# Optimization experiments

Hardware: AMD Instinct MI355X
Metric: run time of the kernel (lower is better)

## Reference

```python
import jax, jax.numpy as jnp
import numpy as np

HIDDEN = 1024
HEADS = 16
HEAD_DIM = HIDDEN // HEADS


def setup_inputs() -> dict:
    key = jax.random.key(0)
    ks = jax.random.split(key, 9)
    s = 1.0 / np.sqrt(HIDDEN)
    x = jax.random.normal(ks[0], (2, 2048, HIDDEN), dtype=jnp.float32)
    Wq = jax.random.uniform(ks[1], (HIDDEN, HIDDEN), jnp.float32, -s, s)
    bq = jax.random.uniform(ks[2], (HIDDEN,), jnp.float32, -s, s)
    Wk = jax.random.uniform(ks[3], (HIDDEN, HIDDEN), jnp.float32, -s, s)
    bk = jax.random.uniform(ks[4], (HIDDEN,), jnp.float32, -s, s)
    Wv = jax.random.uniform(ks[5], (HIDDEN, HIDDEN), jnp.float32, -s, s)
    bv = jax.random.uniform(ks[6], (HIDDEN,), jnp.float32, -s, s)
    Wo = jax.random.uniform(ks[7], (HIDDEN, HIDDEN), jnp.float32, -s, s)
    bo = jax.random.uniform(ks[8], (HIDDEN,), jnp.float32, -s, s)
    return {"x": x, "Wq": Wq, "bq": bq, "Wk": Wk, "bk": bk,
            "Wv": Wv, "bv": bv, "Wo": Wo, "bo": bo}


def reference(x, Wq, bq, Wk, bk, Wv, bv, Wo, bo):
    bs, seq_len, _ = x.shape
    # projections; weights stored as (in, out) so y = x @ W + b
    def proj(W, b):
        y = x @ W + b  # [bs, seq, hidden]
        return y.reshape(bs, seq_len, HEADS, HEAD_DIM).transpose(0, 2, 1, 3)  # [bs, h, seq, hd]
    q = proj(Wq, bq)
    k = proj(Wk, bk)
    v = proj(Wv, bv)
    scale = 1.0 / jnp.sqrt(jnp.float32(HEAD_DIM))
    scores = jnp.einsum('bhqd,bhkd->bhqk', q, k) * scale  # [bs, h, seq, seq]
    attn = jax.nn.softmax(scores, axis=-1)
    ctx = jnp.einsum('bhqk,bhkd->bhqd', attn, v)
    ctx = ctx.transpose(0, 2, 1, 3).reshape(bs, seq_len, HIDDEN)
    return ctx @ Wo + bo
```

## Files before the change

kernel.cpp:

```cpp
#include <hip/hip_runtime.h>
#include <hip/hip_bf16.h>

#define HDN 1024
#define NH  16
#define DH  64
#define NB  2
#define SQL 2048
#define MT  (NB*SQL)

using bf16 = __hip_bfloat16;
typedef __attribute__((ext_vector_type(8))) short s16x8;
typedef __attribute__((ext_vector_type(4))) float f32x4;
typedef __attribute__((ext_vector_type(16))) float f32x16;
typedef unsigned int u32;

#define QSC 0.18033688011112042f

__device__ __forceinline__ void gload_lds16(const void* g, void* l) {
  __builtin_amdgcn_global_load_lds((const __attribute__((address_space(1))) void*)g,
                                   (__attribute__((address_space(3))) void*)l, 16, 0, 0);
}

__device__ __forceinline__ unsigned short bfb(float f) {
  union { __hip_bfloat16 h; unsigned short u; } c;
  c.h = __float2bfloat16(f);
  return c.u;
}

__device__ __forceinline__ u32 cvtpk(float lo, float hi) {
  u32 r;
  asm("v_cvt_pk_bf16_f32 %0, %1, %2" : "=v"(r) : "v"(lo), "v"(hi));
  return r;
}

__device__ __forceinline__ void pl32swap(u32& a, u32& b) {
  asm("v_permlane32_swap_b32 %0, %1" : "+v"(a), "+v"(b));
}

__global__ __launch_bounds__(256) void k_cvt_x(const float* __restrict__ x, bf16* __restrict__ xb) {
  int i = (blockIdx.x * 256 + threadIdx.x) * 8;
  float4 a = *(const float4*)(x + i);
  float4 b = *(const float4*)(x + i + 4);
  union { unsigned short u[8]; uint4 v; } o;
  o.u[0]=bfb(a.x); o.u[1]=bfb(a.y); o.u[2]=bfb(a.z); o.u[3]=bfb(a.w);
  o.u[4]=bfb(b.x); o.u[5]=bfb(b.y); o.u[6]=bfb(b.z); o.u[7]=bfb(b.w);
  *(uint4*)((unsigned short*)xb + i) = o.v;
}

__global__ __launch_bounds__(256) void k_trw(const float* __restrict__ Wq, const float* __restrict__ Wk,
                                             const float* __restrict__ Wv, const float* __restrict__ Wo,
                                             bf16* __restrict__ WqkvT, bf16* __restrict__ WoT) {
  __shared__ float tile[64][65];
  int z = blockIdx.z;
  const float* W = (z==0)?Wq:(z==1)?Wk:(z==2)?Wv:Wo;
  bf16* Wt = (z<3) ? (WqkvT + (size_t)z*HDN*HDN) : WoT;
  int r0 = blockIdx.y*64, c0 = blockIdx.x*64;
  int t = threadIdx.x, tr = t>>4, tc = (t&15)*4;
  #pragma unroll
  for (int p=0;p<4;p++){
    int r = p*16+tr;
    float4 v = *(const float4*)(W + (size_t)(r0+r)*HDN + c0 + tc);
    tile[r][tc]=v.x; tile[r][tc+1]=v.y; tile[r][tc+2]=v.z; tile[r][tc+3]=v.w;
  }
  __syncthreads();
  #pragma unroll
  for (int p=0;p<4;p++){
    int o = p*16+tr;
    union { unsigned short u[4]; ushort4 v; } pk;
    #pragma unroll
    for (int j=0;j<4;j++) pk.u[j] = bfb(tile[tc+j][o]);
    *(ushort4*)((unsigned short*)Wt + (size_t)(c0+o)*HDN + r0 + tc) = pk.v;
  }
}

template<int MODE>
__global__ __launch_bounds__(256,2) void k_gemm(
    const bf16* __restrict__ A, const bf16* __restrict__ B,
    const float* __restrict__ b0, const float* __restrict__ b1, const float* __restrict__ b2,
    bf16* __restrict__ oq, bf16* __restrict__ ok, bf16* __restrict__ ovt, float* __restrict__ oo) {
  constexpr int KD = 1024;
  __shared__ __align__(16) char smem[34816];
  bf16* As = (bf16*)smem;
  bf16* Bs = (bf16*)(smem + 16384);
  int tid = threadIdx.x, lane = tid&63, wave = tid>>6;
  int g = lane>>4, lr = lane&15;

  int lin = blockIdx.y * gridDim.x + blockIdx.x;
  int nwg = gridDim.x * gridDim.y;
  int wg  = (lin & 7) * (nwg >> 3) + (lin >> 3);
  int bx  = wg % gridDim.x, by = wg / gridDim.x;

  int m0 = by*128, n0 = bx*128;
  int wm = (wave>>1)*64, wn = (wave&1)*64;
  f32x4 acc[4][4] = {};
  for (int k0=0; k0<KD; k0+=64) {
    #pragma unroll
    for (int i=0;i<4;i++){
      int seg = wave*4+i;
      int flat = seg*64 + lane;
      int row = flat>>3, ch = flat&7;
      gload_lds16(A + (size_t)(m0+row)*KD + k0 + ch*8, (char*)As + seg*1024);
      gload_lds16(B + (size_t)(n0+row)*KD + k0 + ch*8, (char*)Bs + seg*1024);
    }
    __syncthreads();
    #pragma unroll
    for (int kk=0;kk<2;kk++){
      s16x8 af[4], bfg[4];
      #pragma unroll
      for (int mi=0;mi<4;mi++)
        af[mi] = *(const s16x8*)((const char*)As + (wm+mi*16+lr)*128 + kk*64 + g*16);
      #pragma unroll
      for (int ni=0;ni<4;ni++)
        bfg[ni] = *(const s16x8*)((const char*)Bs + (wn+ni*16+lr)*128 + kk*64 + g*16);
      #pragma unroll
      for (int mi=0;mi<4;mi++)
        #pragma unroll
        for (int ni=0;ni<4;ni++)
          acc[mi][ni] = __builtin_amdgcn_mfma_f32_16x16x32_bf16(af[mi], bfg[ni], acc[mi][ni], 0,0,0);
    }
    __syncthreads();
  }
  if (MODE == 0) {
    int proj = n0 >> 10;
    if (proj < 2) {
      const float* bias = (proj==0)?b0:b1;
      bf16* oqk = (proj==0)?oq:ok;
      float qscale = (proj==0) ? QSC : 1.0f;
      #pragma unroll
      for (int ni=0;ni<4;ni++){
        int n = n0 + wn + ni*16 + lr;
        int wi = n & 1023;
        int h = wi>>6, d = wi&63;
        float bv = bias[wi];
        #pragma unroll
        for (int mi=0;mi<4;mi++){
          #pragma unroll
          for (int r=0;r<4;r++){
            int m = m0 + wm + mi*16 + g*4 + r;
            int b = m>>11, s = m&2047;
            float v = (acc[mi][ni][r] + bv) * qscale;
            oqk[((size_t)((b*NH+h)*SQL + s))*DH + d] = __float2bfloat16(v);
          }
        }
      }
    } else {
      #pragma unroll
      for (int ni=0;ni<4;ni++){
        int nl = wn + ni*16 + lr;
        float bv = b2[(n0 & 1023) + nl];
        #pragma unroll
        for (int mi=0;mi<4;mi++){
          #pragma unroll
          for (int rp=0; rp<4; rp+=2){
            int ml = wm + mi*16 + g*4 + rp;
            u32 pkd = (u32)bfb(acc[mi][ni][rp] + bv) | ((u32)bfb(acc[mi][ni][rp+1] + bv) << 16);
            *(u32*)(smem + nl*272 + ml*2) = pkd;
          }
        }
      }
      __syncthreads();
      int bb = m0 >> 11;
      #pragma unroll
      for (int it=0; it<8; ++it){
        int flat = it*256 + tid;
        int row = flat>>4, chk = flat&15;
        s16x8 val = *(const s16x8*)(smem + row*272 + chk*16);
        int wi = (n0 & 1023) + row;
        int hh = wi>>6, dd = wi&63;
        int ss = (m0 & 2047) + chk*8;
        *(s16x8*)(ovt + ((size_t)((bb*NH+hh)*DH + dd))*SQL + ss) = val;
      }
    }
  } else {
    #pragma unroll
    for (int ni=0;ni<4;ni++){
      int n = n0 + wn + ni*16 + lr;
      float bv = b0[n];
      #pragma unroll
      for (int mi=0;mi<4;mi++)
        #pragma unroll
        for (int r=0;r<4;r++){
          int m = m0 + wm + mi*16 + g*4 + r;
          oo[(size_t)m*HDN + n] = acc[mi][ni][r] + bv;
        }
    }
  }
}

__global__ __launch_bounds__(512,4) void k_attn(
    const bf16* __restrict__ Q, const bf16* __restrict__ K, const bf16* __restrict__ Vt,
    bf16* __restrict__ ctx) {
  __shared__ __align__(16) char sm[2][2][16384];
  int bh = blockIdx.x & 31, qt = blockIdx.x >> 5;
  int b = bh >> 4, h = bh & 15;
  int tid = threadIdx.x;
  int kc = tid >> 8, tl = tid & 255;
  int w4 = tl >> 6;
  int lane = tid & 63;
  int cl = lane & 31, hi = lane >> 5;
  const char* Kc = (const char*)(K  + (size_t)bh*SQL*DH);
  const char* Vc = (const char*)(Vt + (size_t)bh*DH*SQL);
  const bf16* Qb = Q + (size_t)bh*SQL*DH;

  int L0 = tl*16, L1 = 4096 + tl*16;
  int r0 = L0>>7, c0 = (L0&127) ^ ((r0&7)<<4);
  int r1 = L1>>7, c1 = (L1&127) ^ ((r1&7)<<4);
  size_t kOff0 = (size_t)r0*128  + c0, kOff1 = (size_t)r1*128  + c1;
  size_t vOff0 = (size_t)r0*4096 + c0, vOff1 = (size_t)r1*4096 + c1;

  int swz = (cl&7)<<4;
  int cswz0 = (0*32 + hi*16) ^ swz;
  int cswz1 = (1*32 + hi*16) ^ swz;
  int cswz2 = (2*32 + hi*16) ^ swz;
  int cswz3 = (3*32 + hi*16) ^ swz;
  int rbase0 = cl*128;
  int rbase1 = (32+cl)*128;

  int q0 = qt*128 + w4*32;
  s16x8 qf[4];
  #pragma unroll
  for (int ds=0; ds<4; ++ds)
    qf[ds] = *(const s16x8*)((const char*)Qb + (size_t)(q0+cl)*128 + ds*32 + hi*16);

  s16x8 onef;
  #pragma unroll
  for (int i=0;i<8;i++) onef[i] = (short)0x3F80;

  f32x16 ca0 = {}, ca1 = {}, lacc = {};

  auto STAGE = [&](int bb, int t){
    int k0 = kc*1024 + t*64;
    char* bK = &sm[kc][bb][0]; char* bV = bK + 8192;
    gload_lds16(Kc + (size_t)k0*128 + kOff0, bK + w4*1024);
    gload_lds16(Kc + (size_t)k0*128 + kOff1, bK + 4096 + w4*1024);
    gload_lds16(Vc + (size_t)k0*2   + vOff0, bV + w4*1024);
    gload_lds16(Vc + (size_t)k0*2   + vOff1, bV + 4096 + w4*1024);
  };

  STAGE(0, 0);
  __syncthreads();

  for (int t=0; t<16; ++t){
    int cur = t & 1;
    if (t < 15) STAGE(cur^1, t+1);
    const char* bK = &sm[kc][cur][0];
    const char* bV = bK + 8192;

    f32x16 s0 = {}, s1 = {};
    __builtin_amdgcn_s_setprio(1);
    {
      s16x8 k00 = *(const s16x8*)(bK + rbase0 + cswz0);
      s16x8 k10 = *(const s16x8*)(bK + rbase1 + cswz0);
      s0 = __builtin_amdgcn_mfma_f32_32x32x16_bf16(k00, qf[0], s0, 0,0,0);
      s1 = __builtin_amdgcn_mfma_f32_32x32x16_bf16(k10, qf[0], s1, 0,0,0);
      s16x8 k01 = *(const s16x8*)(bK + rbase0 + cswz1);
      s16x8 k11 = *(const s16x8*)(bK + rbase1 + cswz1);
      s0 = __builtin_amdgcn_mfma_f32_32x32x16_bf16(k01, qf[1], s0, 0,0,0);
      s1 = __builtin_amdgcn_mfma_f32_32x32x16_bf16(k11, qf[1], s1, 0,0,0);
      s16x8 k02 = *(const s16x8*)(bK + rbase0 + cswz2);
      s16x8 k12 = *(const s16x8*)(bK + rbase1 + cswz2);
      s0 = __builtin_amdgcn_mfma_f32_32x32x16_bf16(k02, qf[2], s0, 0,0,0);
      s1 = __builtin_amdgcn_mfma_f32_32x32x16_bf16(k12, qf[2], s1, 0,0,0);
      s16x8 k03 = *(const s16x8*)(bK + rbase0 + cswz3);
      s16x8 k13 = *(const s16x8*)(bK + rbase1 + cswz3);
      s0 = __builtin_amdgcn_mfma_f32_32x32x16_bf16(k03, qf[3], s0, 0,0,0);
      s1 = __builtin_amdgcn_mfma_f32_32x32x16_bf16(k13, qf[3], s1, 0,0,0);
    }
    __builtin_amdgcn_s_setprio(0);

    s16x8 pf[4];
    #pragma unroll
    for (int kb=0; kb<2; ++kb){
      float e[16];
      #pragma unroll
      for (int i=0;i<16;i++) e[i] = exp2f(kb ? s1[i] : s0[i]);
      u32 w00=cvtpk(e[0],e[1]),   w01=cvtpk(e[2],e[3]);
      u32 w10=cvtpk(e[4],e[5]),   w11=cvtpk(e[6],e[7]);
      u32 w20=cvtpk(e[8],e[9]),   w21=cvtpk(e[10],e[11]);
      u32 w30=cvtpk(e[12],e[13]), w31=cvtpk(e[14],e[15]);
      pl32swap(w00, w10);
      pl32swap(w01, w11);
      pl32swap(w20, w30);
      pl32swap(w21, w31);
      union { u32 u[4]; s16x8 v; } A, B;
      A.u[0]=w00; A.u[1]=w01; A.u[2]=w10; A.u[3]=w11;
      B.u[0]=w20; B.u[1]=w21; B.u[2]=w30; B.u[3]=w31;
      pf[kb*2]   = A.v;
      pf[kb*2+1] = B.v;
    }

    __builtin_amdgcn_s_setprio(1);
    {
      s16x8 v00 = *(const s16x8*)(bV + rbase0 + cswz0);
      s16x8 v10 = *(const s16x8*)(bV + rbase1 + cswz0);
      ca0 = __builtin_amdgcn_mfma_f32_32x32x16_bf16(v00, pf[0], ca0, 0,0,0);
      ca1 = __builtin_amdgcn_mfma_f32_32x32x16_bf16(v10, pf[0], ca1, 0,0,0);
      lacc = __builtin_amdgcn_mfma_f32_32x32x16_bf16(onef, pf[0], lacc, 0,0,0);
      s16x8 v01 = *(const s16x8*)(bV + rbase0 + cswz1);
      s16x8 v11 = *(const s16x8*)(bV + rbase1 + cswz1);
      ca0 = __builtin_amdgcn_mfma_f32_32x32x16_bf16(v01, pf[1], ca0, 0,0,0);
      ca1 = __builtin_amdgcn_mfma_f32_32x32x16_bf16(v11, pf[1], ca1, 0,0,0);
      lacc = __builtin_amdgcn_mfma_f32_32x32x16_bf16(onef, pf[1], lacc, 0,0,0);
      s16x8 v02 = *(const s16x8*)(bV + rbase0 + cswz2);
      s16x8 v12 = *(const s16x8*)(bV + rbase1 + cswz2);
      ca0 = __builtin_amdgcn_mfma_f32_32x32x16_bf16(v02, pf[2], ca0, 0,0,0);
      ca1 = __builtin_amdgcn_mfma_f32_32x32x16_bf16(v12, pf[2], ca1, 0,0,0);
      lacc = __builtin_amdgcn_mfma_f32_32x32x16_bf16(onef, pf[2], lacc, 0,0,0);
      s16x8 v03 = *(const s16x8*)(bV + rbase0 + cswz3);
      s16x8 v13 = *(const s16x8*)(bV + rbase1 + cswz3);
      ca0 = __builtin_amdgcn_mfma_f32_32x32x16_bf16(v03, pf[3], ca0, 0,0,0);
      ca1 = __builtin_amdgcn_mfma_f32_32x32x16_bf16(v13, pf[3], ca1, 0,0,0);
      lacc = __builtin_amdgcn_mfma_f32_32x32x16_bf16(onef, pf[3], lacc, 0,0,0);
    }
    __builtin_amdgcn_s_setprio(0);
    __syncthreads();
  }

  float lrow = lacc[0];

  char*  base = &sm[0][0][0];
  float* lb   = (float*)(base + 16384);
  float* o2b  = (float*)(base + 32768);
  char*  cb   = base;

  __syncthreads();
  if (kc == 1) {
    if (!hi) lb[w4*32+cl] = lrow;
    #pragma unroll
    for (int db=0; db<2; ++db)
      #pragma unroll
      for (int r=0; r<16; ++r){
        int d = db*32 + (r&3) + 8*(r>>2) + 4*hi;
        o2b[w4*2048 + d*32 + cl] = db ? ca1[r] : ca0[r];
      }
  }
  __syncthreads();
  if (kc == 0) {
    float inv = 1.f / (lrow + lb[w4*32+cl]);
    int row = w4*32 + cl;
    int rswz = (row&7)<<4;
    #pragma unroll
    for (int db=0; db<2; ++db){
      #pragma unroll
      for (int r=0; r<16; r+=2){
        int d = db*32 + (r&3) + 8*(r>>2) + 4*hi;
        float va = ((db?ca1[r]:ca0[r])     + o2b[w4*2048 + d*32     + cl]) * inv;
        float vb = ((db?ca1[r+1]:ca0[r+1]) + o2b[w4*2048 + (d+1)*32 + cl]) * inv;
        *(u32*)(cb + row*128 + ((d*2) ^ rswz)) = cvtpk(va, vb);
      }
    }
  }
  __syncthreads();
  if (kc == 0) {
    #pragma unroll
    for (int i=0;i<4;i++){
      int flat = i*256 + tl, orow = flat>>3, ch = flat&7;
      s16x8 cv = *(const s16x8*)(cb + orow*128 + ((ch*16) ^ ((orow&7)<<4)));
      *(s16x8*)(ctx + (size_t)(b*SQL + qt*128 + orow)*HDN + h*DH + ch*8) = cv;
    }
  }
}

extern "C" void kernel_launch(void* const* d_in, const int* in_sizes, int n_in,
                              void* d_out, int out_size, void* d_ws, size_t ws_size,
                              hipStream_t stream) {
  const float* x  = (const float*)d_in[0];
  const float* Wq = (const float*)d_in[1];
  const float* bq = (const float*)d_in[2];
  const float* Wk = (const float*)d_in[3];
  const float* bk = (const float*)d_in[4];
  const float* Wv = (const float*)d_in[5];
  const float* bv = (const float*)d_in[6];
  const float* Wo = (const float*)d_in[7];
  const float* bo = (const float*)d_in[8];
  char* ws = (char*)d_ws;
  bf16* xb    = (bf16*)(ws);
  bf16* WqkvT = (bf16*)(ws + ((size_t)8<<20));
  bf16* WoT   = (bf16*)(ws + ((size_t)14<<20));
  bf16* Qg    = (bf16*)(ws + ((size_t)16<<20));
  bf16* Kg    = (bf16*)(ws + ((size_t)24<<20));
  bf16* Vtg   = (bf16*)(ws + ((size_t)32<<20));
  bf16* Ctx   = (bf16*)(ws + ((size_t)40<<20));
  float* out  = (float*)d_out;

  k_cvt_x<<<2048, 256, 0, stream>>>(x, xb);
  k_trw<<<dim3(16,16,4), 256, 0, stream>>>(Wq, Wk, Wv, Wo, WqkvT, WoT);
  k_gemm<0><<<dim3(24,32), 256, 0, stream>>>(xb, WqkvT, bq, bk, bv, Qg, Kg, Vtg, nullptr);
  k_attn<<<512, 512, 0, stream>>>(Qg, Kg, Vtg, Ctx);
  k_gemm<1><<<dim3(8,32), 256, 0, stream>>>(Ctx, WoT, bo, nullptr, nullptr,
                                            nullptr, nullptr, nullptr, out);
}
```

Measured before the change: 197.6 us.

## Give each attention wave two Q subtiles, drop ones-MFMA row sums, stage QK epilogue

The attention kernel shrinks to 256 threads, with each wave handling 64 query rows as two 32-row subtiles that share every loaded K/V fragment. This halves LDS fragment reads per MFMA. The ones-matrix MFMA used for row sums is replaced by scalar accumulation of the exponentials plus a cross-half shuffle. Separately, the Q/K projection epilogue now goes through shared memory so it can issue 16-byte coalesced stores instead of scattered 2-byte stores, and the GEMM launch bound asks for 3 blocks per CU. The costs are higher register pressure in attention and fewer threads per block to hide latency.

```diff
diff --git a/kernel.cpp b/kernel.cpp
--- a/kernel.cpp
+++ b/kernel.cpp
@@ -74,7 +74,7 @@
 }
 
 template<int MODE>
-__global__ __launch_bounds__(256,2) void k_gemm(
+__global__ __launch_bounds__(256,3) void k_gemm(
     const bf16* __restrict__ A, const bf16* __restrict__ B,
     const float* __restrict__ b0, const float* __restrict__ b1, const float* __restrict__ b2,
     bf16* __restrict__ oq, bf16* __restrict__ ok, bf16* __restrict__ ovt, float* __restrict__ oo) {
@@ -128,20 +128,27 @@
       float qscale = (proj==0) ? QSC : 1.0f;
       #pragma unroll
       for (int ni=0;ni<4;ni++){
-        int n = n0 + wn + ni*16 + lr;
-        int wi = n & 1023;
-        int h = wi>>6, d = wi&63;
-        float bv = bias[wi];
-        #pragma unroll
-        for (int mi=0;mi<4;mi++){
+        int nl = wn + ni*16 + lr;
+        float bv = bias[(n0&1023) + nl];
+        #pragma unroll
+        for (int mi=0;mi<4;mi++)
           #pragma unroll
           for (int r=0;r<4;r++){
-            int m = m0 + wm + mi*16 + g*4 + r;
-            int b = m>>11, s = m&2047;
-            float v = (acc[mi][ni][r] + bv) * qscale;
-            oqk[((size_t)((b*NH+h)*SQL + s))*DH + d] = __float2bfloat16(v);
+            int ml = wm + mi*16 + g*4 + r;
+            *(unsigned short*)(smem + ml*272 + nl*2) = bfb((acc[mi][ni][r] + bv) * qscale);
           }
-        }
+      }
+      __syncthreads();
+      int bb = m0 >> 11;
+      int h0 = (n0 & 1023) >> 6;
+      #pragma unroll
+      for (int it=0; it<8; ++it){
+        int flat = it*256 + tid;
+        int row = flat>>4, chk = flat&15;
+        s16x8 val = *(const s16x8*)(smem + row*272 + chk*16);
+        int s = (m0 & 2047) + row;
+        int hh = h0 + (chk>>3), dd = (chk&7)*8;
+        *(s16x8*)(oqk + ((size_t)((bb*NH+hh)*SQL + s))*DH + dd) = val;
       }
     } else {
       #pragma unroll
@@ -187,26 +194,25 @@
   }
 }
 
-__global__ __launch_bounds__(512,4) void k_attn(
+__global__ __launch_bounds__(256,2) void k_attn(
     const bf16* __restrict__ Q, const bf16* __restrict__ K, const bf16* __restrict__ Vt,
     bf16* __restrict__ ctx) {
   __shared__ __align__(16) char sm[2][2][16384];
   int bh = blockIdx.x & 31, qt = blockIdx.x >> 5;
   int b = bh >> 4, h = bh & 15;
   int tid = threadIdx.x;
-  int kc = tid >> 8, tl = tid & 255;
-  int w4 = tl >> 6;
+  int kc = tid >> 7, tl = tid & 127;
+  int qw = tl >> 6;
   int lane = tid & 63;
   int cl = lane & 31, hi = lane >> 5;
   const char* Kc = (const char*)(K  + (size_t)bh*SQL*DH);
   const char* Vc = (const char*)(Vt + (size_t)bh*DH*SQL);
   const bf16* Qb = Q + (size_t)bh*SQL*DH;
 
-  int L0 = tl*16, L1 = 4096 + tl*16;
-  int r0 = L0>>7, c0 = (L0&127) ^ ((r0&7)<<4);
-  int r1 = L1>>7, c1 = (L1&127) ^ ((r1&7)<<4);
-  size_t kOff0 = (size_t)r0*128  + c0, kOff1 = (size_t)r1*128  + c1;
-  size_t vOff0 = (size_t)r0*4096 + c0, vOff1 = (size_t)r1*4096 + c1;
+  int r8 = tl >> 3;
+  int cS = ((tl & 7) * 16) ^ ((r8 & 7) << 4);
+  size_t kS = (size_t)r8*128  + cS;
+  size_t vS = (size_t)r8*4096 + cS;
 
   int swz = (cl&7)<<4;
   int cswz0 = (0*32 + hi*16) ^ swz;
@@ -216,25 +222,27 @@
   int rbase0 = cl*128;
   int rbase1 = (32+cl)*128;
 
-  int q0 = qt*128 + w4*32;
-  s16x8 qf[4];
+  int q0 = qt*128 + qw*64;
+  s16x8 qfA[4], qfB[4];
   #pragma unroll
-  for (int ds=0; ds<4; ++ds)
-    qf[ds] = *(const s16x8*)((const char*)Qb + (size_t)(q0+cl)*128 + ds*32 + hi*16);
-
-  s16x8 onef;
-  #pragma unroll
-  for (int i=0;i<8;i++) onef[i] = (short)0x3F80;
-
-  f32x16 ca0 = {}, ca1 = {}, lacc = {};
+  for (int ds=0; ds<4; ++ds){
+    qfA[ds] = *(const s16x8*)((const char*)Qb + (size_t)(q0+cl)*128    + ds*32 + hi*16);
+    qfB[ds] = *(const s16x8*)((const char*)Qb + (size_t)(q0+32+cl)*128 + ds*32 + hi*16);
+  }
+
+  f32x16 caA0 = {}, caA1 = {}, caB0 = {}, caB1 = {};
+  float lrA = 0.f, lrB = 0.f;
 
   auto STAGE = [&](int bb, int t){
     int k0 = kc*1024 + t*64;
     char* bK = &sm[kc][bb][0]; char* bV = bK + 8192;
-    gload_lds16(Kc + (size_t)k0*128 + kOff0, bK + w4*1024);
-    gload_lds16(Kc + (size_t)k0*128 + kOff1, bK + 4096 + w4*1024);
-    gload_lds16(Vc + (size_t)k0*2   + vOff0, bV + w4*1024);
-    gload_lds16(Vc + (size_t)k0*2   + vOff1, bV + 4096 + w4*1024);
+    const char* kp = Kc + (size_t)k0*128 + kS;
+    const char* vp = Vc + (size_t)k0*2   + vS;
+    #pragma unroll
+    for (int p=0; p<4; ++p){
+      gload_lds16(kp + p*2048,          bK + qw*1024 + p*2048);
+      gload_lds16(vp + (size_t)p*65536, bV + qw*1024 + p*2048);
+    }
   };
 
   STAGE(0, 0);
@@ -246,77 +254,98 @@
     const char* bK = &sm[kc][cur][0];
     const char* bV = bK + 8192;
 
-    f32x16 s0 = {}, s1 = {};
+    f32x16 sA0 = {}, sA1 = {}, sB0 = {}, sB1 = {};
     __builtin_amdgcn_s_setprio(1);
     {
       s16x8 k00 = *(const s16x8*)(bK + rbase0 + cswz0);
       s16x8 k10 = *(const s16x8*)(bK + rbase1 + cswz0);
-      s0 = __builtin_amdgcn_mfma_f32_32x32x16_bf16(k00, qf[0], s0, 0,0,0);
-      s1 = __builtin_amdgcn_mfma_f32_32x32x16_bf16(k10, qf[0], s1, 0,0,0);
+      sA0 = __builtin_amdgcn_mfma_f32_32x32x16_bf16(k00, qfA[0], sA0, 0,0,0);
+      sA1 = __builtin_amdgcn_mfma_f32_32x32x16_bf16(k10, qfA[0], sA1, 0,0,0);
+      sB0 = __builtin_amdgcn_mfma_f32_32x32x16_bf16(k00, qfB[0], sB0, 0,0,0);
+      sB1 = __builtin_amdgcn_mfma_f32_32x32x16_bf16(k10, qfB[0], sB1, 0,0,0);
       s16x8 k01 = *(const s16x8*)(bK + rbase0 + cswz1);
       s16x8 k11 = *(const s16x8*)(bK + rbase1 + cswz1);
-      s0 = __builtin_amdgcn_mfma_f32_32x32x16_bf16(k01, qf[1], s0, 0,0,0);
-      s1 = __builtin_amdgcn_mfma_f32_32x32x16_bf16(k11, qf[1], s1, 0,0,0);
+      sA0 = __builtin_amdgcn_mfma_f32_32x32x16_bf16(k01, qfA[1], sA0, 0,0,0);
+      sA1 = __builtin_amdgcn_mfma_f32_32x32x16_bf16(k11, qfA[1], sA1, 0,0,0);
+      sB0 = __builtin_amdgcn_mfma_f32_32x32x16_bf16(k01, qfB[1], sB0, 0,0,0);
+      sB1 = __builtin_amdgcn_mfma_f32_32x32x16_bf16(k11, qfB[1], sB1, 0,0,0);
       s16x8 k02 = *(const s16x8*)(bK + rbase0 + cswz2);
       s16x8 k12 = *(const s16x8*)(bK + rbase1 + cswz2);
-      s0 = __builtin_amdgcn_mfma_f32_32x32x16_bf16(k02, qf[2], s0, 0,0,0);
-      s1 = __builtin_amdgcn_mfma_f32_32x32x16_bf16(k12, qf[2], s1, 0,0,0);
+      sA0 = __builtin_amdgcn_mfma_f32_32x32x16_bf16(k02, qfA[2], sA0, 0,0,0);
+      sA1 = __builtin_amdgcn_mfma_f32_32x32x16_bf16(k12, qfA[2], sA1, 0,0,0);
+      sB0 = __builtin_amdgcn_mfma_f32_32x32x16_bf16(k02, qfB[2], sB0, 0,0,0);
+      sB1 = __builtin_amdgcn_mfma_f32_32x32x16_bf16(k12, qfB[2], sB1, 0,0,0);
       s16x8 k03 = *(const s16x8*)(bK + rbase0 + cswz3);
       s16x8 k13 = *(const s16x8*)(bK + rbase1 + cswz3);
-      s0 = __builtin_amdgcn_mfma_f32_32x32x16_bf16(k03, qf[3], s0, 0,0,0);
-      s1 = __builtin_amdgcn_mfma_f32_32x32x16_bf16(k13, qf[3], s1, 0,0,0);
+      sA0 = __builtin_amdgcn_mfma_f32_32x32x16_bf16(k03, qfA[3], sA0, 0,0,0);
+      sA1 = __builtin_amdgcn_mfma_f32_32x32x16_bf16(k13, qfA[3], sA1, 0,0,0);
+      sB0 = __builtin_amdgcn_mfma_f32_32x32x16_bf16(k03, qfB[3], sB0, 0,0,0);
+      sB1 = __builtin_amdgcn_mfma_f32_32x32x16_bf16(k13, qfB[3], sB1, 0,0,0);
     }
     __builtin_amdgcn_s_setprio(0);
 
-    s16x8 pf[4];
-    #pragma unroll
-    for (int kb=0; kb<2; ++kb){
-      float e[16];
-      #pragma unroll
-      for (int i=0;i<16;i++) e[i] = exp2f(kb ? s1[i] : s0[i]);
-      u32 w00=cvtpk(e[0],e[1]),   w01=cvtpk(e[2],e[3]);
-      u32 w10=cvtpk(e[4],e[5]),   w11=cvtpk(e[6],e[7]);
-      u32 w20=cvtpk(e[8],e[9]),   w21=cvtpk(e[10],e[11]);
-      u32 w30=cvtpk(e[12],e[13]), w31=cvtpk(e[14],e[15]);
-      pl32swap(w00, w10);
-      pl32swap(w01, w11);
-      pl32swap(w20, w30);
-      pl32swap(w21, w31);
-      union { u32 u[4]; s16x8 v; } A, B;
-      A.u[0]=w00; A.u[1]=w01; A.u[2]=w10; A.u[3]=w11;
-      B.u[0]=w20; B.u[1]=w21; B.u[2]=w30; B.u[3]=w31;
-      pf[kb*2]   = A.v;
-      pf[kb*2+1] = B.v;
+    s16x8 pfA[4], pfB[4];
+    #pragma unroll
+    for (int st=0; st<2; ++st){
+      const f32x16& t0 = st ? sB0 : sA0;
+      const f32x16& t1 = st ? sB1 : sA1;
+      float ls = 0.f;
+      s16x8* pf = st ? pfB : pfA;
+      #pragma unroll
+      for (int kb=0; kb<2; ++kb){
+        float e[16];
+        #pragma unroll
+        for (int i=0;i<16;i++){ e[i] = exp2f(kb ? t1[i] : t0[i]); ls += e[i]; }
+        u32 w00=cvtpk(e[0],e[1]),   w01=cvtpk(e[2],e[3]);
+        u32 w10=cvtpk(e[4],e[5]),   w11=cvtpk(e[6],e[7]);
+        u32 w20=cvtpk(e[8],e[9]),   w21=cvtpk(e[10],e[11]);
+        u32 w30=cvtpk(e[12],e[13]), w31=cvtpk(e[14],e[15]);
+        pl32swap(w00, w10);
+        pl32swap(w01, w11);
+        pl32swap(w20, w30);
+        pl32swap(w21, w31);
+        union { u32 u[4]; s16x8 v; } Au, Bu;
+        Au.u[0]=w00; Au.u[1]=w01; Au.u[2]=w10; Au.u[3]=w11;
+        Bu.u[0]=w20; Bu.u[1]=w21; Bu.u[2]=w30; Bu.u[3]=w31;
+        pf[kb*2]   = Au.v;
+        pf[kb*2+1] = Bu.v;
+      }
+      if (st) lrB += ls; else lrA += ls;
     }
 
     __builtin_amdgcn_s_setprio(1);
     {
       s16x8 v00 = *(const s16x8*)(bV + rbase0 + cswz0);
       s16x8 v10 = *(const s16x8*)(bV + rbase1 + cswz0);
-      ca0 = __builtin_amdgcn_mfma_f32_32x32x16_bf16(v00, pf[0], ca0, 0,0,0);
-      ca1 = __builtin_amdgcn_mfma_f32_32x32x16_bf16(v10, pf[0], ca1, 0,0,0);
-      lacc = __builtin_amdgcn_mfma_f32_32x32x16_bf16(onef, pf[0], lacc, 0,0,0);
+      caA0 = __builtin_amdgcn_mfma_f32_32x32x16_bf16(v00, pfA[0], caA0, 0,0,0);
+      caA1 = __builtin_amdgcn_mfma_f32_32x32x16_bf16(v10, pfA[0], caA1, 0,0,0);
+      caB0 = __builtin_amdgcn_mfma_f32_32x32x16_bf16(v00, pfB[0], caB0, 0,0,0);
+      caB1 = __builtin_amdgcn_mfma_f32_32x32x16_bf16(v10, pfB[0], caB1, 0,0,0);
       s16x8 v01 = *(const s16x8*)(bV + rbase0 + cswz1);
       s16x8 v11 = *(const s16x8*)(bV + rbase1 + cswz1);
-      ca0 = __builtin_amdgcn_mfma_f32_32x32x16_bf16(v01, pf[1], ca0, 0,0,0);
-      ca1 = __builtin_amdgcn_mfma_f32_32x32x16_bf16(v11, pf[1], ca1, 0,0,0);
-      lacc = __builtin_amdgcn_mfma_f32_32x32x16_bf16(onef, pf[1], lacc, 0,0,0);
+      caA0 = __builtin_amdgcn_mfma_f32_32x32x16_bf16(v01, pfA[1], caA0, 0,0,0);
+      caA1 = __builtin_amdgcn_mfma_f32_32x32x16_bf16(v11, pfA[1], caA1, 0,0,0);
+      caB0 = __builtin_amdgcn_mfma_f32_32x32x16_bf16(v01, pfB[1], caB0, 0,0,0);
+      caB1 = __builtin_amdgcn_mfma_f32_32x32x16_bf16(v11, pfB[1], caB1, 0,0,0);
       s16x8 v02 = *(const s16x8*)(bV + rbase0 + cswz2);
       s16x8 v12 = *(const s16x8*)(bV + rbase1 + cswz2);
-      ca0 = __builtin_amdgcn_mfma_f32_32x32x16_bf16(v02, pf[2], ca0, 0,0,0);
-      ca1 = __builtin_amdgcn_mfma_f32_32x32x16_bf16(v12, pf[2], ca1, 0,0,0);
-      lacc = __builtin_amdgcn_mfma_f32_32x32x16_bf16(onef, pf[2], lacc, 0,0,0);
+      caA0 = __builtin_amdgcn_mfma_f32_32x32x16_bf16(v02, pfA[2], caA0, 0,0,0);
+      caA1 = __builtin_amdgcn_mfma_f32_32x32x16_bf16(v12, pfA[2], caA1, 0,0,0);
+      caB0 = __builtin_amdgcn_mfma_f32_32x32x16_bf16(v02, pfB[2], caB0, 0,0,0);
+      caB1 = __builtin_amdgcn_mfma_f32_32x32x16_bf16(v12, pfB[2], caB1, 0,0,0);
       s16x8 v03 = *(const s16x8*)(bV + rbase0 + cswz3);
       s16x8 v13 = *(const s16x8*)(bV + rbase1 + cswz3);
-      ca0 = __builtin_amdgcn_mfma_f32_32x32x16_bf16(v03, pf[3], ca0, 0,0,0);
-      ca1 = __builtin_amdgcn_mfma_f32_32x32x16_bf16(v13, pf[3], ca1, 0,0,0);
-      lacc = __builtin_amdgcn_mfma_f32_32x32x16_bf16(onef, pf[3], lacc, 0,0,0);
+      caA0 = __builtin_amdgcn_mfma_f32_32x32x16_bf16(v03, pfA[3], caA0, 0,0,0);
+      caA1 = __builtin_amdgcn_mfma_f32_32x32x16_bf16(v13, pfA[3], caA1, 0,0,0);
+      caB0 = __builtin_amdgcn_mfma_f32_32x32x16_bf16(v03, pfB[3], caB0, 0,0,0);
+      caB1 = __builtin_amdgcn_mfma_f32_32x32x16_bf16(v13, pfB[3], caB1, 0,0,0);
     }
     __builtin_amdgcn_s_setprio(0);
     __syncthreads();
   }
 
-  float lrow = lacc[0];
+  lrA += __shfl_xor(lrA, 32, 64);
+  lrB += __shfl_xor(lrB, 32, 64);
 
   char*  base = &sm[0][0][0];
   float* lb   = (float*)(base + 16384);
@@ -325,36 +354,48 @@
 
   __syncthreads();
   if (kc == 1) {
-    if (!hi) lb[w4*32+cl] = lrow;
-    #pragma unroll
-    for (int db=0; db<2; ++db)
-      #pragma unroll
-      for (int r=0; r<16; ++r){
-        int d = db*32 + (r&3) + 8*(r>>2) + 4*hi;
-        o2b[w4*2048 + d*32 + cl] = db ? ca1[r] : ca0[r];
-      }
+    if (!hi) { lb[(qw*2+0)*32+cl] = lrA; lb[(qw*2+1)*32+cl] = lrB; }
+    #pragma unroll
+    for (int st=0; st<2; ++st){
+      int su = qw*2 + st;
+      #pragma unroll
+      for (int db=0; db<2; ++db)
+        #pragma unroll
+        for (int r=0; r<16; ++r){
+          int d = db*32 + (r&3) + 8*(r>>2) + 4*hi;
+          float v = st ? (db ? caB1[r] : caB0[r]) : (db ? caA1[r] : caA0[r]);
+          o2b[su*2048 + d*32 + cl] = v;
+        }
+    }
   }
   __syncthreads();
   if (kc == 0) {
-    float inv = 1.f / (lrow + lb[w4*32+cl]);
-    int row = w4*32 + cl;
-    int rswz = (row&7)<<4;
-    #pragma unroll
-    for (int db=0; db<2; ++db){
-      #pragma unroll
-      for (int r=0; r<16; r+=2){
-        int d = db*32 + (r&3) + 8*(r>>2) + 4*hi;
-        float va = ((db?ca1[r]:ca0[r])     + o2b[w4*2048 + d*32     + cl]) * inv;
-        float vb = ((db?ca1[r+1]:ca0[r+1]) + o2b[w4*2048 + (d+1)*32 + cl]) * inv;
-        *(u32*)(cb + row*128 + ((d*2) ^ rswz)) = cvtpk(va, vb);
+    #pragma unroll
+    for (int st=0; st<2; ++st){
+      int su = qw*2 + st;
+      float lr = st ? lrB : lrA;
+      float inv = 1.f / (lr + lb[su*32+cl]);
+      int row = su*32 + cl;
+      int rswz = (row&7)<<4;
+      #pragma unroll
+      for (int db=0; db<2; ++db){
+        #pragma unroll
+        for (int r=0; r<16; r+=2){
+          int d = db*32 + (r&3) + 8*(r>>2) + 4*hi;
+          float sa = st ? (db ? caB1[r]   : caB0[r])   : (db ? caA1[r]   : caA0[r]);
+          float sb = st ? (db ? caB1[r+1] : caB0[r+1]) : (db ? caA1[r+1] : caA0[r+1]);
+          float va = (sa + o2b[su*2048 + d*32     + cl]) * inv;
+          float vb = (sb + o2b[su*2048 + (d+1)*32 + cl]) * inv;
+          *(u32*)(cb + row*128 + ((d*2) ^ rswz)) = cvtpk(va, vb);
+        }
       }
     }
   }
   __syncthreads();
   if (kc == 0) {
     #pragma unroll
-    for (int i=0;i<4;i++){
-      int flat = i*256 + tl, orow = flat>>3, ch = flat&7;
+    for (int i=0;i<8;i++){
+      int flat = i*128 + tl, orow = flat>>3, ch = flat&7;
       s16x8 cv = *(const s16x8*)(cb + orow*128 + ((ch*16) ^ ((orow&7)<<4)));
       *(s16x8*)(ctx + (size_t)(b*SQL + qt*128 + orow)*HDN + h*DH + ch*8) = cv;
     }
@@ -386,7 +427,7 @@
   k_cvt_x<<<2048, 256, 0, stream>>>(x, xb);
   k_trw<<<dim3(16,16,4), 256, 0, stream>>>(Wq, Wk, Wv, Wo, WqkvT, WoT);
   k_gemm<0><<<dim3(24,32), 256, 0, stream>>>(xb, WqkvT, bq, bk, bv, Qg, Kg, Vtg, nullptr);
-  k_attn<<<512, 512, 0, stream>>>(Qg, Kg, Vtg, Ctx);
+  k_attn<<<512, 256, 0, stream>>>(Qg, Kg, Vtg, Ctx);
   k_gemm<1><<<dim3(8,32), 256, 0, stream>>>(Ctx, WoT, bo, nullptr, nullptr,
                                             nullptr, nullptr, nullptr, out);
 }
```

Result: slower. 204.9 us (+3.7%).
